# Kernel tuning notes

Hardware: AMD Instinct MI355X
Metric: run time of the kernel (lower is better)

Reference implementation:

```python
import jax, jax.numpy as jnp
import numpy as np

B, JX, JQ, D = 16, 4096, 512, 256
VERY_NEG = -1e30


def setup_inputs() -> dict:
    key = jax.random.key(0)
    ks = jax.random.split(key, 8)
    c = jax.random.normal(ks[0], (B, JX, D), dtype=jnp.float32)
    q = jax.random.normal(ks[1], (B, JQ, D), dtype=jnp.float32)
    # glorot-ish scaled weights for [4d, d] projections
    s = 1.0 / np.sqrt(4 * D)
    Wr = jax.random.normal(ks[2], (4 * D, D), dtype=jnp.float32) * s
    Wg = jax.random.normal(ks[3], (4 * D, D), dtype=jnp.float32) * s
    Br = jnp.zeros((D,), dtype=jnp.float32)
    Bg = jnp.zeros((D,), dtype=jnp.float32)
    # padding masks from random valid lengths (realistic ragged batch)
    c_len = jax.random.randint(ks[4], (B,), JX // 2, JX + 1)
    q_len = jax.random.randint(ks[5], (B,), JQ // 2, JQ + 1)
    c_mask = jnp.arange(JX)[None, :] < c_len[:, None]
    q_mask = jnp.arange(JQ)[None, :] < q_len[:, None]
    return {"c": c, "q": q, "Wr": Wr, "Br": Br, "Wg": Wg, "Bg": Bg,
            "c_mask": c_mask, "q_mask": q_mask}


def reference(c, q, Wr, Br, Wg, Bg, c_mask, q_mask):
    # logits[b,x,j] = <c[b,x], q[b,j]>
    logits = jnp.einsum('bxd,bjd->bxj', c, q)
    # exp_mask: add VERY_NEG where (c_mask & q_mask) is False
    cq_mask = c_mask[:, :, None] & q_mask[:, None, :]  # [B,JX,JQ]
    logits = logits + (1.0 - cq_mask.astype(logits.dtype)) * VERY_NEG
    a = jax.nn.softmax(logits, axis=-1)                # [B,JX,JQ]
    q_a = jnp.einsum('bxj,bjd->bxd', a, q)             # [B,JX,D]
    # semantic fusion unit
    cc = jnp.concatenate([c, q_a, c * q_a, c - q_a], axis=-1)  # [B,JX,4D]
    r_ = jnp.tanh(cc @ Wr + Br)
    g = jax.nn.sigmoid(cc @ Wg + Bg)
    return g * r_ + (1.0 - g) * c
```

## Files before the change

kernel.cpp:

```cpp
#include <hip/hip_runtime.h>
#include <hip/hip_bf16.h>
#include <stdint.h>

#define NB 16
#define JXX 4096
#define JQQ 512
#define DDD 256
#define LOG2E 1.44269504f

typedef __attribute__((ext_vector_type(8))) _Float16 f16x8;
typedef __attribute__((ext_vector_type(4))) _Float16 f16x4;
typedef __attribute__((ext_vector_type(4))) float f32x4;

__device__ __forceinline__ uint16_t f2h(float f) {
    union { _Float16 h; uint16_t s; } u; u.h = (_Float16)f; return u.s;
}

__device__ __forceinline__ void gload_lds16(const void* g, void* l) {
    __builtin_amdgcn_global_load_lds(
        (const __attribute__((address_space(1))) void*)g,
        (__attribute__((address_space(3))) void*)l, 16, 0, 0);
}

__global__ void k_mask(const void* cmask, const void* qmask,
                       uint8_t* cm8, uint8_t* qm8) {
    int i = blockIdx.x * 256 + threadIdx.x;
    uint32_t w0c = *(const uint32_t*)cmask;
    uint32_t w0q = *(const uint32_t*)qmask;
    int mc = (w0c == 1u) ? 1 : (w0c == 0x3f800000u ? 2 : 0);
    int mq = (w0q == 1u) ? 1 : (w0q == 0x3f800000u ? 2 : 0);
    if (i < NB * JXX) {
        uint8_t v;
        if (mc == 1)      v = ((const int*)cmask)[i] != 0;
        else if (mc == 2) v = ((const float*)cmask)[i] != 0.0f;
        else              v = ((const uint8_t*)cmask)[i] != 0;
        cm8[i] = v;
    }
    if (i < NB * JQQ) {
        uint8_t v;
        if (mq == 1)      v = ((const int*)qmask)[i] != 0;
        else if (mq == 2) v = ((const float*)qmask)[i] != 0.0f;
        else              v = ((const uint8_t*)qmask)[i] != 0;
        qm8[i] = v;
    }
}

__global__ void k_prep_q(const float* __restrict__ qg,
                         uint16_t* __restrict__ qS,
                         uint16_t* __restrict__ qTS) {
    __shared__ float tile[64][65];
    const int b = blockIdx.z, j0 = blockIdx.x * 64, d0 = blockIdx.y * 64;
    const int t = threadIdx.x;
    #pragma unroll
    for (int i = 0; i < 16; i++) {
        int e = t + 256 * i;
        int r = e >> 6, c = e & 63;
        tile[r][c] = qg[((long)b * JQQ + j0 + r) * DDD + d0 + c];
    }
    __syncthreads();
    #pragma unroll
    for (int i = 0; i < 2; i++) {
        int e = t + 256 * i;
        int r = e >> 3, c8 = e & 7;
        f16x8 v;
        #pragma unroll
        for (int k = 0; k < 8; k++) v[k] = (_Float16)tile[r][c8 * 8 + k];
        int jt = (j0 >> 5) + (r >> 5);
        int row = r & 31;
        int d8 = (d0 >> 3) + c8;
        int byt = ((row * 512 + d8 * 16) ^ ((row & 7) << 4));
        *(f16x8*)(qS + ((long)(b * 16 + jt)) * 8192 + (byt >> 1)) = v;
    }
    #pragma unroll
    for (int i = 0; i < 2; i++) {
        int e = t + 256 * i;
        int dd = e >> 3, j8 = e & 7;
        f16x8 v;
        #pragma unroll
        for (int k = 0; k < 8; k++) v[k] = (_Float16)tile[j8 * 8 + k][dd];
        int jt = (j0 >> 5) + (j8 >> 2);
        int d = d0 + dd;
        int byt = ((d * 64 + (j8 & 3) * 16) ^ (((d >> 1) & 3) << 4));
        *(f16x8*)(qTS + ((long)(b * 16 + jt)) * 8192 + (byt >> 1)) = v;
    }
}

__global__ void k_prep_w(const float* __restrict__ Wr, const float* __restrict__ Wg,
                         uint16_t* __restrict__ WrP, uint16_t* __restrict__ WgP) {
    __shared__ _Float16 tile[32 * 264];
    const float* W = blockIdx.y ? Wg : Wr;
    uint16_t* WP = blockIdx.y ? WgP : WrP;
    const int kt = blockIdx.x, t = threadIdx.x;
    #pragma unroll
    for (int i = 0; i < 32; i++) {
        int e = t + 256 * i;
        int r = e >> 8, c = e & 255;
        tile[r * 264 + c] = (_Float16)W[(long)(kt * 32 + r) * 256 + c];
    }
    __syncthreads();
    #pragma unroll
    for (int ss = 0; ss < 4; ss++) {
        int slot = ss * 256 + t;
        int nt = slot >> 6, lane = slot & 63;
        int gg = lane >> 4, l = lane & 15;
        f16x8 v;
        #pragma unroll
        for (int i = 0; i < 8; i++) v[i] = tile[(gg * 8 + i) * 264 + nt * 16 + l];
        *(f16x8*)(WP + ((long)(kt * 16 + nt) * 64 + lane) * 8) = v;
    }
}

__global__ __launch_bounds__(256, 2) void k_attn(
    const float* __restrict__ cg,
    const uint16_t* __restrict__ qS,
    const uint16_t* __restrict__ qTS,
    const uint8_t* __restrict__ cm8,
    const uint8_t* __restrict__ qm8,
    uint16_t* __restrict__ qa16)
{
    __shared__ __align__(16) uint16_t qbuf[2][8192];
    __shared__ __align__(16) uint16_t qTbuf[2][8192];
    __shared__ __align__(16) uint16_t P_lds[4 * 32 * 40];
    __shared__ __align__(16) uint32_t qm_lds[128];

    const int b = blockIdx.y;
    const int t = threadIdx.x;
    const int wave = t >> 6;
    const int lane = t & 63;
    const int l15 = lane & 15;
    const int g = lane >> 4;
    const int xw = blockIdx.x * 128 + wave * 32;

    if (t < 128) {
        uint32_t m = ((const uint32_t*)(qm8 + (long)b * JQQ))[t];
        qm_lds[t] = m;
    }

    f16x8 cfrag[2][8];
    bool cvalid[2];
    float m_run[2], s_run[2];
    #pragma unroll
    for (int xs = 0; xs < 2; xs++) {
        const float* crow = cg + ((long)b * JXX + xw + xs * 16 + l15) * DDD;
        #pragma unroll
        for (int kb = 0; kb < 8; kb++) {
            float4 v0 = *(const float4*)(crow + kb * 32 + g * 8);
            float4 v1 = *(const float4*)(crow + kb * 32 + g * 8 + 4);
            f16x8 f;
            f[0] = (_Float16)v0.x; f[1] = (_Float16)v0.y; f[2] = (_Float16)v0.z; f[3] = (_Float16)v0.w;
            f[4] = (_Float16)v1.x; f[5] = (_Float16)v1.y; f[6] = (_Float16)v1.z; f[7] = (_Float16)v1.w;
            cfrag[xs][kb] = f;
        }
        cvalid[xs] = cm8[(long)b * JXX + xw + xs * 16 + l15] != 0;
        m_run[xs] = cvalid[xs] ? -1e30f : 0.0f;
        s_run[xs] = 0.0f;
    }
    const f32x4 fzero = {0.f, 0.f, 0.f, 0.f};
    f32x4 qa[16][2];
    #pragma unroll
    for (int i = 0; i < 16; i++) { qa[i][0] = fzero; qa[i][1] = fzero; }

    const uint16_t* qSb  = qS  + (long)(b * 16) * 8192;
    const uint16_t* qTSb = qTS + (long)(b * 16) * 8192;

    const int kbit = (l15 >> 2) & 1;
    const int qbase = l15 * 256 + (((g * 16) ^ ((l15 & 3) << 4)) >> 1);
    const int qTbase = l15 * 32 + ((g ^ ((l15 >> 1) & 3)) * 8);

    #define STAGE_ATTN(bsel, tile)                                              \
        {                                                                       \
            const uint16_t* s1 = qSb + (long)(tile) * 8192;                     \
            const uint16_t* s2 = qTSb + (long)(tile) * 8192;                    \
            _Pragma("unroll")                                                   \
            for (int i = 0; i < 4; i++)                                         \
                gload_lds16(s1 + i * 2048 + t * 8,                              \
                            &qbuf[bsel][i * 2048 + wave * 512]);                \
            _Pragma("unroll")                                                   \
            for (int i = 0; i < 4; i++)                                         \
                gload_lds16(s2 + i * 2048 + t * 8,                              \
                            &qTbuf[bsel][i * 2048 + wave * 512]);               \
        }

    STAGE_ATTN(0, 0);
    asm volatile("s_waitcnt lgkmcnt(0)" ::: "memory");
    __builtin_amdgcn_s_barrier();

    int cur = 0;
    for (int jt = 0; jt < 16; jt++) {
        if (jt < 15) {
            STAGE_ATTN(cur ^ 1, jt + 1);
            asm volatile("s_waitcnt vmcnt(8)" ::: "memory");
        } else {
            asm volatile("s_waitcnt vmcnt(0)" ::: "memory");
        }
        __builtin_amdgcn_s_barrier();
        __builtin_amdgcn_sched_barrier(0);

        const uint16_t* qb_l  = &qbuf[cur][0];
        const uint16_t* qTb_l = &qTbuf[cur][0];

        uint32_t qmw[2];
        qmw[0] = qm_lds[jt * 8 + g];
        qmw[1] = qm_lds[jt * 8 + 4 + g];

        f32x4 acc[2][2];
        acc[0][0] = fzero; acc[0][1] = fzero; acc[1][0] = fzero; acc[1][1] = fzero;
        #pragma unroll
        for (int js = 0; js < 2; js++) {
            #pragma unroll
            for (int kb = 0; kb < 8; kb++) {
                f16x8 qf = *(const f16x8*)(qb_l + js * 4096 + qbase + ((kb ^ kbit) << 5));
                acc[js][0] = __builtin_amdgcn_mfma_f32_16x16x32_f16(qf, cfrag[0][kb], acc[js][0], 0, 0, 0);
                acc[js][1] = __builtin_amdgcn_mfma_f32_16x16x32_f16(qf, cfrag[1][kb], acc[js][1], 0, 0, 0);
            }
        }

        f16x4 pv[2][2];
        float fsc[2];
        #pragma unroll
        for (int xs = 0; xs < 2; xs++) {
            float lmax = -1e30f;
            #pragma unroll
            for (int js = 0; js < 2; js++) {
                #pragma unroll
                for (int r = 0; r < 4; r++) {
                    bool qv = (qmw[js] >> (8 * r)) & 0xffu;
                    lmax = fmaxf(lmax, qv ? acc[js][xs][r] : -1e30f);
                }
            }
            lmax = fmaxf(lmax, __shfl_xor(lmax, 16));
            lmax = fmaxf(lmax, __shfl_xor(lmax, 32));
            float m_new = cvalid[xs] ? fmaxf(m_run[xs], lmax) : 0.0f;
            fsc[xs] = exp2f((m_run[xs] - m_new) * LOG2E);
            float psum = 0.0f;
            #pragma unroll
            for (int js = 0; js < 2; js++) {
                #pragma unroll
                for (int r = 0; r < 4; r++) {
                    bool qv = (qmw[js] >> (8 * r)) & 0xffu;
                    float p = qv ? exp2f((acc[js][xs][r] - m_new) * LOG2E) : 0.0f;
                    if (!cvalid[xs]) p = 1.0f;
                    psum += p;
                    pv[xs][js][r] = (_Float16)p;
                }
            }
            s_run[xs] = s_run[xs] * fsc[xs] + psum;
            m_run[xs] = m_new;
        }
        if (!__all(fsc[0] == 1.0f && fsc[1] == 1.0f)) {
            #pragma unroll
            for (int dt = 0; dt < 16; dt++) {
                #pragma unroll
                for (int xs = 0; xs < 2; xs++) {
                    qa[dt][xs][0] *= fsc[xs]; qa[dt][xs][1] *= fsc[xs];
                    qa[dt][xs][2] *= fsc[xs]; qa[dt][xs][3] *= fsc[xs];
                }
            }
        }

        uint16_t* Pw0 = P_lds + wave * 1280;
        #pragma unroll
        for (int xs = 0; xs < 2; xs++) {
            *(f16x4*)(Pw0 + (xs * 16 + l15) * 40 + g * 4) = pv[xs][0];
            *(f16x4*)(Pw0 + (xs * 16 + l15) * 40 + 16 + g * 4) = pv[xs][1];
        }
        f16x8 pa[2];
        pa[0] = *(const f16x8*)(Pw0 + l15 * 40 + g * 8);
        pa[1] = *(const f16x8*)(Pw0 + (16 + l15) * 40 + g * 8);

        #pragma unroll
        for (int dt = 0; dt < 16; dt++) {
            f16x8 bq = *(const f16x8*)(qTb_l + qTbase + dt * 512);
            qa[dt][0] = __builtin_amdgcn_mfma_f32_16x16x32_f16(bq, pa[0], qa[dt][0], 0, 0, 0);
            qa[dt][1] = __builtin_amdgcn_mfma_f32_16x16x32_f16(bq, pa[1], qa[dt][1], 0, 0, 0);
        }

        __builtin_amdgcn_sched_barrier(0);
        __builtin_amdgcn_s_barrier();
        cur ^= 1;
    }
    #undef STAGE_ATTN

    #pragma unroll
    for (int xs = 0; xs < 2; xs++) {
        float s_tot = s_run[xs] + __shfl_xor(s_run[xs], 16);
        s_tot = s_tot + __shfl_xor(s_tot, 32);
        float inv = 1.0f / s_tot;
        uint16_t* outp = qa16 + ((long)b * JXX + xw + xs * 16 + l15) * DDD;
        #pragma unroll
        for (int dt = 0; dt < 16; dt++) {
            f16x4 v;
            v[0] = (_Float16)(qa[dt][xs][0] * inv);
            v[1] = (_Float16)(qa[dt][xs][1] * inv);
            v[2] = (_Float16)(qa[dt][xs][2] * inv);
            v[3] = (_Float16)(qa[dt][xs][3] * inv);
            *(f16x4*)(outp + dt * 16 + g * 4) = v;
        }
    }
}

__global__ __launch_bounds__(256, 3) void k_sfu(
    const float* __restrict__ cg,
    const uint16_t* __restrict__ qa16,
    const uint16_t* __restrict__ WrP,
    const uint16_t* __restrict__ WgP,
    const float* __restrict__ Brb,
    const float* __restrict__ Bgb,
    float* __restrict__ outg)
{
    __shared__ __align__(16) uint16_t c_lds[64 * 72];
    __shared__ __align__(16) uint16_t qa_lds[64 * 72];
    __shared__ __align__(16) uint16_t wbuf[2][8192];

    const int t = threadIdx.x;
    const int wave = t >> 6;
    const int lane = t & 63;
    const int l15 = lane & 15, g = lane >> 4;
    const int mw = wave & 1, nw = wave >> 1;
    const long m0 = (long)blockIdx.x * 64;
    const int n0 = blockIdx.y * 128, ny0 = blockIdx.y * 8;

    const f32x4 fzero = {0.f, 0.f, 0.f, 0.f};
    f32x4 accR[2][4], accG[2][4];
    #pragma unroll
    for (int a = 0; a < 2; a++)
        #pragma unroll
        for (int bq = 0; bq < 4; bq++) { accR[a][bq] = fzero; accG[a][bq] = fzero; }

    #define STAGE_W(bufp, kt)                                                     \
        {                                                                         \
            _Pragma("unroll")                                                     \
            for (int i = 0; i < 4; i++) {                                         \
                int s = i * 4 + wave;                                             \
                const uint16_t* src = (s < 8)                                     \
                    ? WrP + ((long)((kt) * 16 + ny0 + s) * 64 + lane) * 8         \
                    : WgP + ((long)((kt) * 16 + ny0 + s - 8) * 64 + lane) * 8;    \
                gload_lds16(src, (bufp) + i * 2048 + wave * 512);                 \
            }                                                                     \
        }

    int cur = 0;
    STAGE_W(&wbuf[0][0], 0);

    #pragma unroll
    for (int dt = 0; dt < 4; dt++) {
        __syncthreads();
        #pragma unroll
        for (int i = 0; i < 2; i++) {
            int e = t + 256 * i;
            int row = e >> 3, c8 = e & 7;
            const float* p = cg + (m0 + row) * DDD + dt * 64 + c8 * 8;
            float4 v0 = *(const float4*)p;
            float4 v1 = *(const float4*)(p + 4);
            f16x8 f;
            f[0] = (_Float16)v0.x; f[1] = (_Float16)v0.y; f[2] = (_Float16)v0.z; f[3] = (_Float16)v0.w;
            f[4] = (_Float16)v1.x; f[5] = (_Float16)v1.y; f[6] = (_Float16)v1.z; f[7] = (_Float16)v1.w;
            *(f16x8*)(c_lds + row * 72 + c8 * 8) = f;
            *(f16x8*)(qa_lds + row * 72 + c8 * 8) =
                *(const f16x8*)(qa16 + (m0 + row) * DDD + dt * 64 + c8 * 8);
        }
        __syncthreads();
        #pragma unroll
        for (int kb = 0; kb < 2; kb++) {
            f16x8 af[4][2];
            #pragma unroll
            for (int mf = 0; mf < 2; mf++) {
                int row = mw * 32 + mf * 16 + l15;
                f16x8 cf = *(const f16x8*)(c_lds + row * 72 + kb * 32 + g * 8);
                f16x8 qf = *(const f16x8*)(qa_lds + row * 72 + kb * 32 + g * 8);
                af[0][mf] = cf;
                af[1][mf] = qf;
                af[2][mf] = cf * qf;
                af[3][mf] = cf - qf;
            }
            #pragma unroll
            for (int comp = 0; comp < 4; comp++) {
                const int step = (dt * 2 + kb) * 4 + comp;
                if (step < 31) {
                    const int ns = step + 1;
                    const int ndt = ns >> 3, nkb = (ns >> 2) & 1, ncomp = ns & 3;
                    const int nkt = ncomp * 8 + ndt * 2 + nkb;
                    STAGE_W(&wbuf[cur ^ 1][0], nkt);
                    asm volatile("s_waitcnt vmcnt(4)" ::: "memory");
                } else {
                    asm volatile("s_waitcnt vmcnt(0)" ::: "memory");
                }
                __builtin_amdgcn_s_barrier();
                __builtin_amdgcn_sched_barrier(0);
                const uint16_t* Wb = &wbuf[cur][0];
                #pragma unroll
                for (int nt = 0; nt < 4; nt++) {
                    f16x8 br = *(const f16x8*)(Wb + (nw * 4 + nt) * 512 + lane * 8);
                    f16x8 bg = *(const f16x8*)(Wb + 4096 + (nw * 4 + nt) * 512 + lane * 8);
                    accR[0][nt] = __builtin_amdgcn_mfma_f32_16x16x32_f16(af[comp][0], br, accR[0][nt], 0, 0, 0);
                    accR[1][nt] = __builtin_amdgcn_mfma_f32_16x16x32_f16(af[comp][1], br, accR[1][nt], 0, 0, 0);
                    accG[0][nt] = __builtin_amdgcn_mfma_f32_16x16x32_f16(af[comp][0], bg, accG[0][nt], 0, 0, 0);
                    accG[1][nt] = __builtin_amdgcn_mfma_f32_16x16x32_f16(af[comp][1], bg, accG[1][nt], 0, 0, 0);
                }
                __builtin_amdgcn_sched_barrier(0);
                __builtin_amdgcn_s_barrier();
                cur ^= 1;
            }
        }
    }
    #undef STAGE_W

    #pragma unroll
    for (int nt = 0; nt < 4; nt++) {
        int n = n0 + nw * 64 + nt * 16 + l15;
        float br = Brb[n], bg = Bgb[n];
        #pragma unroll
        for (int mf = 0; mf < 2; mf++) {
            long rowb = m0 + mw * 32 + mf * 16 + g * 4;
            #pragma unroll
            for (int r = 0; r < 4; r++) {
                float pr = accR[mf][nt][r] + br;
                float pg = accG[mf][nt][r] + bg;
                float x = fminf(fmaxf(pr, -30.f), 30.f);
                float e2 = __expf(2.f * x);
                float rr = (e2 - 1.f) / (e2 + 1.f);
                float gv = 1.0f / (1.0f + __expf(-pg));
                float cv = cg[(rowb + r) * DDD + n];
                outg[(rowb + r) * DDD + n] = gv * rr + (1.f - gv) * cv;
            }
        }
    }
}

extern "C" void kernel_launch(void* const* d_in, const int* in_sizes, int n_in,
                              void* d_out, int out_size, void* d_ws, size_t ws_size,
                              hipStream_t stream) {
    const float* c  = (const float*)d_in[0];
    const float* q  = (const float*)d_in[1];
    const float* Wr = (const float*)d_in[2];
    const float* Br = (const float*)d_in[3];
    const float* Wg = (const float*)d_in[4];
    const float* Bg = (const float*)d_in[5];
    const void* cmask = d_in[6];
    const void* qmask = d_in[7];

    char* ws = (char*)d_ws;
    uint16_t* qS    = (uint16_t*)(ws + 0);
    uint16_t* qTS   = (uint16_t*)(ws + 4194304);
    uint16_t* qa16  = (uint16_t*)(ws + 8388608);
    uint16_t* WrP   = (uint16_t*)(ws + 41943040);
    uint16_t* WgP   = (uint16_t*)(ws + 42467328);
    uint8_t*  cm8   = (uint8_t*)(ws + 42991616);
    uint8_t*  qm8   = (uint8_t*)(ws + 43057152);
    (void)in_sizes; (void)n_in; (void)out_size; (void)ws_size;

    k_mask<<<dim3((NB * JXX + 255) / 256), dim3(256), 0, stream>>>(cmask, qmask, cm8, qm8);
    k_prep_q<<<dim3(8, 4, NB), dim3(256), 0, stream>>>(q, qS, qTS);
    k_prep_w<<<dim3(32, 2), dim3(256), 0, stream>>>(Wr, Wg, WrP, WgP);
    k_attn<<<dim3(JXX / 128, NB), dim3(256), 0, stream>>>(c, qS, qTS, cm8, qm8, qa16);
    k_sfu<<<dim3((NB * JXX) / 64, 2), dim3(256), 0, stream>>>(
        c, qa16, WrP, WgP, Br, Bg, (float*)d_out);
}
```

Before: 168.8 us.

## Stage fp16 c copy and async-load SFU operands with triple-buffered weights

The attention kernel now also writes an fp16 copy of c, so the SFU kernel can stream c and q_a tiles into swizzled LDS with async global-to-LDS loads instead of synchronous fp32 loads and conversions. The weights are repacked into a step-ordered layout, and the SFU kernel uses a triple-buffered weight pipeline with prefetch two steps ahead. The aim is to remove the per-dt __syncthreads stalls and halve c traffic in the SFU. In exchange it adds a 32MB fp16 write in k_attn, lowers SFU occupancy to 2 blocks, and the final residual now uses the fp16-rounded c, which loses precision.

```diff
diff --git a/kernel.cpp b/kernel.cpp
--- a/kernel.cpp
+++ b/kernel.cpp
@@ -15,12 +15,17 @@
 __device__ __forceinline__ uint16_t f2h(float f) {
     union { _Float16 h; uint16_t s; } u; u.h = (_Float16)f; return u.s;
 }
+__device__ __forceinline__ float h2f(uint16_t s) {
+    union { _Float16 h; uint16_t s; } u; u.s = s; return (float)u.h;
+}
 
 __device__ __forceinline__ void gload_lds16(const void* g, void* l) {
     __builtin_amdgcn_global_load_lds(
         (const __attribute__((address_space(1))) void*)g,
         (__attribute__((address_space(3))) void*)l, 16, 0, 0);
 }
+
+#define VMW(N) asm volatile("s_waitcnt vmcnt(" #N ")" ::: "memory")
 
 __global__ void k_mask(const void* cmask, const void* qmask,
                        uint8_t* cm8, uint8_t* qm8) {
@@ -86,10 +91,10 @@
 }
 
 __global__ void k_prep_w(const float* __restrict__ Wr, const float* __restrict__ Wg,
-                         uint16_t* __restrict__ WrP, uint16_t* __restrict__ WgP) {
+                         uint16_t* __restrict__ WP2) {
     __shared__ _Float16 tile[32 * 264];
-    const float* W = blockIdx.y ? Wg : Wr;
-    uint16_t* WP = blockIdx.y ? WgP : WrP;
+    const int rg = blockIdx.y;
+    const float* W = rg ? Wg : Wr;
     const int kt = blockIdx.x, t = threadIdx.x;
     #pragma unroll
     for (int i = 0; i < 32; i++) {
@@ -98,15 +103,18 @@
         tile[r * 264 + c] = (_Float16)W[(long)(kt * 32 + r) * 256 + c];
     }
     __syncthreads();
+    const int step = (kt & 7) * 4 + (kt >> 3);
     #pragma unroll
     for (int ss = 0; ss < 4; ss++) {
         int slot = ss * 256 + t;
-        int nt = slot >> 6, lane = slot & 63;
+        int ntg = slot >> 6, lane = slot & 63;
         int gg = lane >> 4, l = lane & 15;
         f16x8 v;
         #pragma unroll
-        for (int i = 0; i < 8; i++) v[i] = tile[(gg * 8 + i) * 264 + nt * 16 + l];
-        *(f16x8*)(WP + ((long)(kt * 16 + nt) * 64 + lane) * 8) = v;
+        for (int i = 0; i < 8; i++) v[i] = tile[(gg * 8 + i) * 264 + ntg * 16 + l];
+        int hh = ntg >> 3, ntl = ntg & 7;
+        long off = (long)step * 16384 + hh * 8192 + rg * 4096 + ntl * 512 + lane * 8;
+        *(f16x8*)(WP2 + off) = v;
     }
 }
 
@@ -116,7 +124,8 @@
     const uint16_t* __restrict__ qTS,
     const uint8_t* __restrict__ cm8,
     const uint8_t* __restrict__ qm8,
-    uint16_t* __restrict__ qa16)
+    uint16_t* __restrict__ qa16,
+    uint16_t* __restrict__ c16)
 {
     __shared__ __align__(16) uint16_t qbuf[2][8192];
     __shared__ __align__(16) uint16_t qTbuf[2][8192];
@@ -141,7 +150,9 @@
     float m_run[2], s_run[2];
     #pragma unroll
     for (int xs = 0; xs < 2; xs++) {
-        const float* crow = cg + ((long)b * JXX + xw + xs * 16 + l15) * DDD;
+        const long rowg = (long)b * JXX + xw + xs * 16 + l15;
+        const float* crow = cg + rowg * DDD;
+        uint16_t* c16row = c16 + rowg * DDD;
         #pragma unroll
         for (int kb = 0; kb < 8; kb++) {
             float4 v0 = *(const float4*)(crow + kb * 32 + g * 8);
@@ -150,8 +161,9 @@
             f[0] = (_Float16)v0.x; f[1] = (_Float16)v0.y; f[2] = (_Float16)v0.z; f[3] = (_Float16)v0.w;
             f[4] = (_Float16)v1.x; f[5] = (_Float16)v1.y; f[6] = (_Float16)v1.z; f[7] = (_Float16)v1.w;
             cfrag[xs][kb] = f;
-        }
-        cvalid[xs] = cm8[(long)b * JXX + xw + xs * 16 + l15] != 0;
+            *(f16x8*)(c16row + kb * 32 + g * 8) = f;
+        }
+        cvalid[xs] = cm8[rowg] != 0;
         m_run[xs] = cvalid[xs] ? -1e30f : 0.0f;
         s_run[xs] = 0.0f;
     }
@@ -189,9 +201,9 @@
     for (int jt = 0; jt < 16; jt++) {
         if (jt < 15) {
             STAGE_ATTN(cur ^ 1, jt + 1);
-            asm volatile("s_waitcnt vmcnt(8)" ::: "memory");
+            VMW(8);
         } else {
-            asm volatile("s_waitcnt vmcnt(0)" ::: "memory");
+            VMW(0);
         }
         __builtin_amdgcn_s_barrier();
         __builtin_amdgcn_sched_barrier(0);
@@ -299,26 +311,25 @@
     }
 }
 
-__global__ __launch_bounds__(256, 3) void k_sfu(
-    const float* __restrict__ cg,
+__global__ __launch_bounds__(256, 2) void k_sfu(
+    const uint16_t* __restrict__ c16g,
     const uint16_t* __restrict__ qa16,
-    const uint16_t* __restrict__ WrP,
-    const uint16_t* __restrict__ WgP,
+    const uint16_t* __restrict__ WP2,
     const float* __restrict__ Brb,
     const float* __restrict__ Bgb,
     float* __restrict__ outg)
 {
-    __shared__ __align__(16) uint16_t c_lds[64 * 72];
-    __shared__ __align__(16) uint16_t qa_lds[64 * 72];
-    __shared__ __align__(16) uint16_t wbuf[2][8192];
+    __shared__ __align__(16) uint16_t ab_lds[2][4096];
+    __shared__ __align__(16) uint16_t wbuf[3][8192];
 
     const int t = threadIdx.x;
-    const int wave = t >> 6;
-    const int lane = t & 63;
+    const int wave = t >> 6, lane = t & 63;
     const int l15 = lane & 15, g = lane >> 4;
     const int mw = wave & 1, nw = wave >> 1;
     const long m0 = (long)blockIdx.x * 64;
-    const int n0 = blockIdx.y * 128, ny0 = blockIdx.y * 8;
+    const int h = blockIdx.y, n0 = h * 128;
+
+    const uint16_t* WPh = WP2 + (long)h * 8192;
 
     const f32x4 fzero = {0.f, 0.f, 0.f, 0.f};
     f32x4 accR[2][4], accG[2][4];
@@ -327,47 +338,43 @@
         #pragma unroll
         for (int bq = 0; bq < 4; bq++) { accR[a][bq] = fzero; accG[a][bq] = fzero; }
 
-    #define STAGE_W(bufp, kt)                                                     \
-        {                                                                         \
-            _Pragma("unroll")                                                     \
-            for (int i = 0; i < 4; i++) {                                         \
-                int s = i * 4 + wave;                                             \
-                const uint16_t* src = (s < 8)                                     \
-                    ? WrP + ((long)((kt) * 16 + ny0 + s) * 64 + lane) * 8         \
-                    : WgP + ((long)((kt) * 16 + ny0 + s - 8) * 64 + lane) * 8;    \
-                gload_lds16(src, (bufp) + i * 2048 + wave * 512);                 \
-            }                                                                     \
-        }
-
-    int cur = 0;
-    STAGE_W(&wbuf[0][0], 0);
+    #define STAGE_CQA(dt_)                                                        \
+        { _Pragma("unroll")                                                       \
+          for (int j = 0; j < 2; j++) {                                           \
+              int pp = j * 256 + t;                                               \
+              int row = pp >> 3, pc = pp & 7;                                     \
+              long src = (m0 + row) * 256 + (dt_) * 64 + ((pc ^ (row & 7)) << 3); \
+              int dst = (j * 256 + wave * 64) * 8;                                \
+              gload_lds16(c16g + src, &ab_lds[0][dst]);                           \
+              gload_lds16(qa16 + src, &ab_lds[1][dst]);                           \
+          } }
+
+    #define STAGE_W(sidx_)                                                        \
+        { _Pragma("unroll")                                                       \
+          for (int i = 0; i < 4; i++) {                                           \
+              int s = i * 4 + wave;                                               \
+              gload_lds16(WPh + (long)(sidx_) * 16384 + s * 512 + lane * 8,       \
+                          &wbuf[(sidx_) % 3][i * 2048 + wave * 512]);             \
+          } }
+
+    STAGE_CQA(0);
+    STAGE_W(0);
+    STAGE_W(1);
+    VMW(8);
+    __builtin_amdgcn_s_barrier();
 
     #pragma unroll
     for (int dt = 0; dt < 4; dt++) {
-        __syncthreads();
-        #pragma unroll
-        for (int i = 0; i < 2; i++) {
-            int e = t + 256 * i;
-            int row = e >> 3, c8 = e & 7;
-            const float* p = cg + (m0 + row) * DDD + dt * 64 + c8 * 8;
-            float4 v0 = *(const float4*)p;
-            float4 v1 = *(const float4*)(p + 4);
-            f16x8 f;
-            f[0] = (_Float16)v0.x; f[1] = (_Float16)v0.y; f[2] = (_Float16)v0.z; f[3] = (_Float16)v0.w;
-            f[4] = (_Float16)v1.x; f[5] = (_Float16)v1.y; f[6] = (_Float16)v1.z; f[7] = (_Float16)v1.w;
-            *(f16x8*)(c_lds + row * 72 + c8 * 8) = f;
-            *(f16x8*)(qa_lds + row * 72 + c8 * 8) =
-                *(const f16x8*)(qa16 + (m0 + row) * DDD + dt * 64 + c8 * 8);
-        }
-        __syncthreads();
         #pragma unroll
         for (int kb = 0; kb < 2; kb++) {
             f16x8 af[4][2];
             #pragma unroll
             for (int mf = 0; mf < 2; mf++) {
                 int row = mw * 32 + mf * 16 + l15;
-                f16x8 cf = *(const f16x8*)(c_lds + row * 72 + kb * 32 + g * 8);
-                f16x8 qf = *(const f16x8*)(qa_lds + row * 72 + kb * 32 + g * 8);
+                int c8 = kb * 4 + g;
+                int off = row * 64 + ((c8 ^ (row & 7)) << 3);
+                f16x8 cf = *(const f16x8*)(&ab_lds[0][off]);
+                f16x8 qf = *(const f16x8*)(&ab_lds[1][off]);
                 af[0][mf] = cf;
                 af[1][mf] = qf;
                 af[2][mf] = cf * qf;
@@ -375,19 +382,17 @@
             }
             #pragma unroll
             for (int comp = 0; comp < 4; comp++) {
-                const int step = (dt * 2 + kb) * 4 + comp;
-                if (step < 31) {
-                    const int ns = step + 1;
-                    const int ndt = ns >> 3, nkb = (ns >> 2) & 1, ncomp = ns & 3;
-                    const int nkt = ncomp * 8 + ndt * 2 + nkb;
-                    STAGE_W(&wbuf[cur ^ 1][0], nkt);
-                    asm volatile("s_waitcnt vmcnt(4)" ::: "memory");
-                } else {
-                    asm volatile("s_waitcnt vmcnt(0)" ::: "memory");
-                }
+                const int sidx = (dt * 2 + kb) * 4 + comp;
+                if (dt < 3 && kb == 1 && comp == 1) STAGE_CQA(dt + 1);
+                if (sidx <= 29) STAGE_W(sidx + 2);
+                if (sidx <= 29) {
+                    if (dt < 3 && kb == 1 && (comp == 1 || comp == 2)) { VMW(12); }
+                    else { VMW(8); }
+                } else if (sidx == 30) { VMW(4); }
+                else { VMW(0); }
                 __builtin_amdgcn_s_barrier();
                 __builtin_amdgcn_sched_barrier(0);
-                const uint16_t* Wb = &wbuf[cur][0];
+                const uint16_t* Wb = &wbuf[sidx % 3][0];
                 #pragma unroll
                 for (int nt = 0; nt < 4; nt++) {
                     f16x8 br = *(const f16x8*)(Wb + (nw * 4 + nt) * 512 + lane * 8);
@@ -399,11 +404,11 @@
                 }
                 __builtin_amdgcn_sched_barrier(0);
                 __builtin_amdgcn_s_barrier();
-                cur ^= 1;
             }
         }
     }
     #undef STAGE_W
+    #undef STAGE_CQA
 
     #pragma unroll
     for (int nt = 0; nt < 4; nt++) {
@@ -420,7 +425,7 @@
                 float e2 = __expf(2.f * x);
                 float rr = (e2 - 1.f) / (e2 + 1.f);
                 float gv = 1.0f / (1.0f + __expf(-pg));
-                float cv = cg[(rowb + r) * DDD + n];
+                float cv = h2f(c16g[(rowb + r) * DDD + n]);
                 outg[(rowb + r) * DDD + n] = gv * rr + (1.f - gv) * cv;
             }
         }
@@ -443,16 +448,16 @@
     uint16_t* qS    = (uint16_t*)(ws + 0);
     uint16_t* qTS   = (uint16_t*)(ws + 4194304);
     uint16_t* qa16  = (uint16_t*)(ws + 8388608);
-    uint16_t* WrP   = (uint16_t*)(ws + 41943040);
-    uint16_t* WgP   = (uint16_t*)(ws + 42467328);
-    uint8_t*  cm8   = (uint8_t*)(ws + 42991616);
-    uint8_t*  qm8   = (uint8_t*)(ws + 43057152);
+    uint16_t* c16   = (uint16_t*)(ws + 41943040);
+    uint16_t* WP2   = (uint16_t*)(ws + 75497472);
+    uint8_t*  cm8   = (uint8_t*)(ws + 77594624);
+    uint8_t*  qm8   = (uint8_t*)(ws + 77660160);
     (void)in_sizes; (void)n_in; (void)out_size; (void)ws_size;
 
     k_mask<<<dim3((NB * JXX + 255) / 256), dim3(256), 0, stream>>>(cmask, qmask, cm8, qm8);
     k_prep_q<<<dim3(8, 4, NB), dim3(256), 0, stream>>>(q, qS, qTS);
-    k_prep_w<<<dim3(32, 2), dim3(256), 0, stream>>>(Wr, Wg, WrP, WgP);
-    k_attn<<<dim3(JXX / 128, NB), dim3(256), 0, stream>>>(c, qS, qTS, cm8, qm8, qa16);
+    k_prep_w<<<dim3(32, 2), dim3(256), 0, stream>>>(Wr, Wg, WP2);
+    k_attn<<<dim3(JXX / 128, NB), dim3(256), 0, stream>>>(c, qS, qTS, cm8, qm8, qa16, c16);
     k_sfu<<<dim3((NB * JXX) / 64, 2), dim3(256), 0, stream>>>(
-        c, qa16, WrP, WgP, Br, Bg, (float*)d_out);
-}
+        c16, qa16, WP2, Br, Bg, (float*)d_out);
+}
```

Result: no change. 171.0 us (+1.4%).
